# Performance work log

Hardware: AMD Instinct MI355X
Metric: run time of the kernel (lower is better)

The kernel has to match this reference:

```python
import jax, jax.numpy as jnp
import numpy as np

D_MODEL = 1024
NHEAD = 16
D_K = D_MODEL // NHEAD


def setup_inputs() -> dict:
    key = jax.random.key(0)
    ks = jax.random.split(key, 9)
    B, S = 2, 2048
    std = 1.0 / np.sqrt(D_MODEL)
    x = jax.random.normal(ks[0], (B, S, D_MODEL), dtype=jnp.float32)
    Wq = jax.random.uniform(ks[1], (D_MODEL, D_MODEL), jnp.float32, -std, std)
    bq = jax.random.uniform(ks[2], (D_MODEL,), jnp.float32, -std, std)
    Wk = jax.random.uniform(ks[3], (D_MODEL, D_MODEL), jnp.float32, -std, std)
    bk = jax.random.uniform(ks[4], (D_MODEL,), jnp.float32, -std, std)
    Wv = jax.random.uniform(ks[5], (D_MODEL, D_MODEL), jnp.float32, -std, std)
    bv = jax.random.uniform(ks[6], (D_MODEL,), jnp.float32, -std, std)
    Wo = jax.random.uniform(ks[7], (D_MODEL, D_MODEL), jnp.float32, -std, std)
    bo = jax.random.uniform(ks[8], (D_MODEL,), jnp.float32, -std, std)
    return {"x": x, "Wq": Wq, "bq": bq, "Wk": Wk, "bk": bk,
            "Wv": Wv, "bv": bv, "Wo": Wo, "bo": bo}


def reference(x, Wq, bq, Wk, bk, Wv, bv, Wo, bo):
    B, S, _ = x.shape
    scale = jnp.float32(np.sqrt(D_K))
    # Linear layers (torch nn.Linear: y = x @ W.T + b; here W stored as [in,out])
    q = (x @ Wq + bq).reshape(B, S, NHEAD, D_K).transpose(0, 2, 1, 3)  # [B,H,S,Dk]
    k = (x @ Wk + bk).reshape(B, S, NHEAD, D_K).transpose(0, 2, 1, 3)
    v = (x @ Wv + bv).reshape(B, S, NHEAD, D_K).transpose(0, 2, 1, 3)
    scores = jnp.einsum('bhqd,bhkd->bhqk', q, k) / scale  # [B,H,S,S]
    attn = jax.nn.softmax(scores, axis=-1)
    # dropout is identity in eval / deterministic reference
    out = jnp.einsum('bhqk,bhkd->bhqd', attn, v)  # [B,H,S,Dk]
    out = out.transpose(0, 2, 1, 3).reshape(B, S, D_MODEL)
    return out @ Wo + bo
```

## Files before the change

### kernel.cpp

```cpp
#include <hip/hip_runtime.h>
#include <math.h>

#define DM    1024
#define NH    16
#define DK    64
#define SLEN  2048
#define NB    2
#define MROWS (NB*SLEN)
#define QSCALE 0.1803368801111204f

typedef unsigned short u16;
typedef unsigned int   u32;
typedef short  s16x8 __attribute__((ext_vector_type(8)));
typedef _Float16 f16x8 __attribute__((ext_vector_type(8)));
typedef float  f32x4  __attribute__((ext_vector_type(4)));
typedef float  f32x16 __attribute__((ext_vector_type(16)));

#define MFMA_F16(a,b,c)   __builtin_amdgcn_mfma_f32_16x16x32_f16(a,b,c,0,0,0)
#define MFMA32_F16(a,b,c) __builtin_amdgcn_mfma_f32_32x32x16_f16(a,b,c,0,0,0)

__device__ __forceinline__ void gload16(const void* g, void* l) {
    __builtin_amdgcn_global_load_lds((const __attribute__((address_space(1))) void*)g,
                                     (__attribute__((address_space(3))) void*)l, 16, 0, 0);
}
__device__ __forceinline__ f16x8 as_h(s16x8 v) {
    union { s16x8 s; f16x8 h; } u; u.s = v; return u.h;
}
__device__ __forceinline__ float exp2_hw(float x) {
    float r; asm("v_exp_f32 %0, %1" : "=v"(r) : "v"(x)); return r;
}
__device__ __forceinline__ u32 pk2(float a, float b) {
    union { _Float16 h[2]; u32 u; } x;
    x.h[0] = (_Float16)a; x.h[1] = (_Float16)b;
    return x.u;
}
__device__ __forceinline__ void pl32swap(u32& a, u32& b) {
    asm volatile("v_permlane32_swap_b32 %0, %1" : "+v"(a), "+v"(b));
}
#define VMCNT0() asm volatile("s_waitcnt vmcnt(0)" ::: "memory")
#define BAR()    __builtin_amdgcn_s_barrier()

__global__ __launch_bounds__(256) void cvt_all(
    const float* __restrict__ x,
    const float* __restrict__ Wq, const float* __restrict__ Wk,
    const float* __restrict__ Wv, const float* __restrict__ Wo,
    _Float16* __restrict__ xh, _Float16* __restrict__ wqkv, _Float16* __restrict__ wo) {
    const int z = blockIdx.z;
    const int t = threadIdx.x;
    if (z == 4) {
        int base = (blockIdx.y * 16 + blockIdx.x) * 256 + t;
#pragma unroll
        for (int u = 0; u < 16; ++u) {
            int i = (base + u * 65536) * 4;
            float4 v = *(const float4*)&x[i];
            float vv[4] = {v.x, v.y, v.z, v.w};
            _Float16 hv[4];
#pragma unroll
            for (int j = 0; j < 4; ++j) hv[j] = (_Float16)vv[j];
            *(ushort4*)&xh[i] = *(ushort4*)hv;
        }
        return;
    }
    __shared__ _Float16 ts[64][72];
    const float* W = (z == 0) ? Wq : (z == 1) ? Wk : (z == 2) ? Wv : Wo;
    _Float16* dst = (z < 3) ? (wqkv + (size_t)z * DM * DM) : wo;
    int k0 = blockIdx.x * 64, n0 = blockIdx.y * 64;
    int kr = t >> 4, c4 = (t & 15) * 4;
#pragma unroll
    for (int u = 0; u < 4; ++u) {
        int k = kr + u * 16;
        float4 v = *(const float4*)&W[(size_t)(k0 + k) * DM + n0 + c4];
        float vv[4] = {v.x, v.y, v.z, v.w};
#pragma unroll
        for (int j = 0; j < 4; ++j) ts[c4 + j][k] = (_Float16)vv[j];
    }
    __syncthreads();
#pragma unroll
    for (int u = 0; u < 4; ++u) {
        int n = kr + u * 16;
        _Float16 hv[4];
#pragma unroll
        for (int j = 0; j < 4; ++j) hv[j] = ts[n][c4 + j];
        *(ushort4*)&dst[(size_t)(n0 + n) * DM + k0 + c4] = *(ushort4*)hv;
    }
}

template<int EPI, int BN_>
__global__ __launch_bounds__(256) void gemm_f16(
    const u16* __restrict__ Ah, const u16* __restrict__ Bt,
    const float* __restrict__ b0, const float* __restrict__ b1, const float* __restrict__ b2,
    float* __restrict__ outf, _Float16* __restrict__ qf,
    _Float16* __restrict__ kfp, _Float16* __restrict__ vtp)
{
    constexpr int NJ = BN_ / 32;
    __shared__ __align__(16) u16 sAh[2][4096];
    __shared__ __align__(16) u16 sB[2][BN_ * 32];
    const int tid = threadIdx.x, wid = tid >> 6, lane = tid & 63;
    const int lq = lane & 15, lk = lane >> 4;
    const int wm = wid >> 1, wn = wid & 1;
    const int bm = blockIdx.x * 128, bn = blockIdx.y * BN_;

    const f32x4 fz = {0.f, 0.f, 0.f, 0.f};
    f32x4 acc[4][NJ];
#pragma unroll
    for (int i = 0; i < 4; ++i)
#pragma unroll
        for (int j = 0; j < NJ; ++j) acc[i][j] = fz;

    auto stage = [&](int b, int k0) {
#pragma unroll
        for (int u = 0; u < 2; ++u) {
            int idx = u * 256 + tid, row = idx >> 2, c = (idx & 3) ^ ((row >> 1) & 3);
            size_t ga = (size_t)(bm + row) * DM + k0 + c * 8;
            gload16(Ah + ga, (char*)&sAh[b][0] + (u * 256 + wid * 64) * 16);
        }
#pragma unroll
        for (int u = 0; u < BN_ / 64; ++u) {
            int idx = u * 256 + tid, row = idx >> 2, c = (idx & 3) ^ ((row >> 1) & 3);
            size_t gb = (size_t)(bn + row) * DM + k0 + c * 8;
            gload16(Bt + gb, (char*)&sB[b][0] + (u * 256 + wid * 64) * 16);
        }
    };
    auto compute = [&](int b) {
        s16x8 avh[4], bv[NJ];
#pragma unroll
        for (int i = 0; i < 4; ++i) {
            int row = wm * 64 + i * 16 + lq;
            int off = row * 32 + ((lk ^ ((row >> 1) & 3)) << 3);
            avh[i] = *(const s16x8*)&sAh[b][off];
        }
#pragma unroll
        for (int j = 0; j < NJ; ++j) {
            int row = wn * (BN_ / 2) + j * 16 + lq;
            int off = row * 32 + ((lk ^ ((row >> 1) & 3)) << 3);
            bv[j] = *(const s16x8*)&sB[b][off];
        }
        __builtin_amdgcn_s_setprio(1);
#pragma unroll
        for (int i = 0; i < 4; ++i)
#pragma unroll
            for (int j = 0; j < NJ; ++j)
                acc[i][j] = MFMA_F16(as_h(avh[i]), as_h(bv[j]), acc[i][j]);
        __builtin_amdgcn_s_setprio(0);
    };

    int buf = 0;
    stage(0, 0);
    VMCNT0(); BAR();
    for (int t = 0; t < 31; ++t) {
        stage(buf ^ 1, (t + 1) * 32);
        compute(buf);
        VMCNT0(); BAR();
        buf ^= 1;
    }
    compute(buf);

#pragma unroll
    for (int j = 0; j < NJ; ++j) {
        int n = bn + wn * (BN_ / 2) + j * 16 + lq;
        if constexpr (EPI == 0) {
            float bias = b0[n];
#pragma unroll
            for (int i = 0; i < 4; ++i)
#pragma unroll
                for (int r = 0; r < 4; ++r) {
                    int m = bm + wm * 64 + i * 16 + lk * 4 + r;
                    outf[(size_t)m * DM + n] = acc[i][j][r] + bias;
                }
        } else {
            int mat = n >> 10, nl = n & 1023;
            int h_ = nl >> 6, d = nl & 63;
            const float* bp = (mat == 0) ? b0 : ((mat == 1) ? b1 : b2);
            float bias = bp[nl];
#pragma unroll
            for (int i = 0; i < 4; ++i) {
                int m0 = bm + wm * 64 + i * 16 + lk * 4;
                int b_ = m0 >> 11, s0 = m0 & (SLEN - 1);
                if (mat == 2) {
                    _Float16 v4[4];
#pragma unroll
                    for (int r = 0; r < 4; ++r) v4[r] = (_Float16)(acc[i][j][r] + bias);
                    *(ushort4*)&vtp[((size_t)(b_ * NH + h_) * DK + d) * SLEN + s0] = *(ushort4*)v4;
                } else {
                    _Float16* dst = (mat == 0) ? qf : kfp;
                    float sc = (mat == 0) ? QSCALE : 1.0f;
#pragma unroll
                    for (int r = 0; r < 4; ++r)
                        dst[((size_t)(b_ * NH + h_) * SLEN + s0 + r) * DK + d] =
                            (_Float16)((acc[i][j][r] + bias) * sc);
                }
            }
        }
    }
}

__global__ __launch_bounds__(256, 2) void attn_mfma(
    const _Float16* __restrict__ qf, const _Float16* __restrict__ kf,
    const _Float16* __restrict__ vt, _Float16* __restrict__ aoh)
{
    __shared__ __align__(16) _Float16 Ks[2][128 * 64];
    __shared__ __align__(16) _Float16 Vs[2][64 * 128];
    const int tid = threadIdx.x, wid = tid >> 6, lane = tid & 63;
    const int ln = lane & 31, l5 = lane >> 5;
    const int phys = blockIdx.x;
    const int virt = (phys & 7) * 64 + (phys >> 3);
    const int bh = virt >> 4, qb = virt & 15;
    const int qrow = qb * 128 + wid * 32 + ln;

    f16x8 qv[4];
#pragma unroll
    for (int t = 0; t < 4; ++t)
        qv[t] = *(const f16x8*)&qf[((size_t)bh * SLEN + qrow) * DK + t * 16 + l5 * 8];

    const _Float16* kbase = kf + (size_t)bh * SLEN * DK;
    const _Float16* vbase = vt + (size_t)bh * DK * SLEN;

    f32x16 O[2];
#pragma unroll
    for (int db = 0; db < 2; ++db)
#pragma unroll
        for (int r = 0; r < 16; ++r) O[db][r] = 0.f;
    float la0 = 0.f, la1 = 0.f, la2 = 0.f, la3 = 0.f;

    auto stage = [&](int b, int t) {
#pragma unroll
        for (int u = 0; u < 4; ++u) {
            int idx = u * 256 + tid, row = idx >> 3, c = (idx & 7) ^ (row & 7);
            gload16(kbase + (size_t)(t * 128 + row) * DK + c * 8,
                    (char*)&Ks[b][0] + (u * 256 + wid * 64) * 16);
        }
#pragma unroll
        for (int u = 0; u < 4; ++u) {
            int idx = u * 256 + tid, row = idx >> 4, c = (idx & 15) ^ (row & 15);
            gload16(vbase + (size_t)row * SLEN + t * 128 + c * 8,
                    (char*)&Vs[b][0] + (u * 256 + wid * 64) * 16);
        }
    };

    auto compute = [&](int b) {
        f32x16 S[4];
        __builtin_amdgcn_s_setprio(1);
#pragma unroll
        for (int kb = 0; kb < 4; ++kb) {
            f32x16 s;
#pragma unroll
            for (int r = 0; r < 16; ++r) s[r] = 0.f;
            int krow = kb * 32 + ln;
#pragma unroll
            for (int tp = 0; tp < 4; ++tp) {
                int cd = (2 * tp + l5) ^ (krow & 7);
                f16x8 ka = *(const f16x8*)&Ks[b][krow * 64 + cd * 8];
                s = MFMA32_F16(ka, qv[tp], s);
            }
            S[kb] = s;
        }
        __builtin_amdgcn_s_setprio(0);

        u32 pk_[4][8];
#pragma unroll
        for (int kb = 0; kb < 4; ++kb) {
#pragma unroll
            for (int i = 0; i < 8; ++i) {
                float p0 = exp2_hw(S[kb][2 * i]);
                float p1 = exp2_hw(S[kb][2 * i + 1]);
                switch (i & 3) {
                    case 0: la0 += p0 + p1; break;
                    case 1: la1 += p0 + p1; break;
                    case 2: la2 += p0 + p1; break;
                    default: la3 += p0 + p1; break;
                }
                pk_[kb][i] = pk2(p0, p1);
            }
            pl32swap(pk_[kb][0], pk_[kb][2]);
            pl32swap(pk_[kb][1], pk_[kb][3]);
            pl32swap(pk_[kb][4], pk_[kb][6]);
            pl32swap(pk_[kb][5], pk_[kb][7]);
        }

        __builtin_amdgcn_s_setprio(1);
#pragma unroll
        for (int kb = 0; kb < 4; ++kb)
#pragma unroll
            for (int t2 = 0; t2 < 2; ++t2) {
                union { u32 w[4]; f16x8 v; } pb;
#pragma unroll
                for (int w = 0; w < 4; ++w) pb.w[w] = pk_[kb][t2 * 4 + w];
#pragma unroll
                for (int db = 0; db < 2; ++db) {
                    int drow = db * 32 + ln;
                    int cd = (kb * 4 + t2 * 2 + l5) ^ (drow & 15);
                    f16x8 va = *(const f16x8*)&Vs[b][drow * 128 + cd * 8];
                    O[db] = MFMA32_F16(va, pb.v, O[db]);
                }
            }
        __builtin_amdgcn_s_setprio(0);
    };

    int buf = 0;
    stage(0, 0);
    VMCNT0(); BAR();
    for (int t = 0; t < SLEN / 128 - 1; ++t) {
        stage(buf ^ 1, t + 1);
        compute(buf);
        VMCNT0(); BAR();
        buf ^= 1;
    }
    compute(buf);

    float lp = (la0 + la1) + (la2 + la3);
    lp += __shfl_xor(lp, 32);
    float inv = 1.0f / lp;
    const int b_ = bh >> 4, h_ = bh & 15;
    size_t rowbase = ((size_t)(b_ * SLEN + qrow)) * DM + h_ * 64;
#pragma unroll
    for (int db = 0; db < 2; ++db)
#pragma unroll
        for (int u = 0; u < 4; ++u) {
            int dbase = 8 * u + 4 * l5 + 32 * db;
            _Float16 h4[4];
#pragma unroll
            for (int j = 0; j < 4; ++j) h4[j] = (_Float16)(O[db][4 * u + j] * inv);
            *(ushort4*)&aoh[rowbase + dbase] = *(ushort4*)h4;
        }
}

extern "C" void kernel_launch(void* const* d_in, const int* in_sizes, int n_in,
                              void* d_out, int out_size, void* d_ws, size_t ws_size,
                              hipStream_t stream) {
    const float* x  = (const float*)d_in[0];
    const float* Wq = (const float*)d_in[1];
    const float* bq = (const float*)d_in[2];
    const float* Wk = (const float*)d_in[3];
    const float* bk = (const float*)d_in[4];
    const float* Wv = (const float*)d_in[5];
    const float* bv = (const float*)d_in[6];
    const float* Wo = (const float*)d_in[7];
    const float* bo = (const float*)d_in[8];
    float* out = (float*)d_out;

    if (ws_size < (size_t)40 * 1024 * 1024) return;
    char* W = (char*)d_ws;
    _Float16* xh   = (_Float16*)(W);
    _Float16* wqkv = (_Float16*)(W + ((size_t)8  << 20));
    _Float16* wo   = (_Float16*)(W + ((size_t)14 << 20));
    _Float16* qf   = (_Float16*)(W + ((size_t)16 << 20));
    _Float16* kf   = (_Float16*)(W + ((size_t)24 << 20));
    _Float16* vt   = (_Float16*)(W + ((size_t)32 << 20));
    _Float16* aoh  = xh;

    cvt_all<<<dim3(16, 16, 5), dim3(256), 0, stream>>>(
        x, Wq, Wk, Wv, Wo, xh, wqkv, wo);

    gemm_f16<1, 128><<<dim3(32, 24), dim3(256), 0, stream>>>(
        (const u16*)xh, (const u16*)wqkv,
        bq, bk, bv, nullptr, qf, kf, vt);

    attn_mfma<<<dim3(512), dim3(256), 0, stream>>>(qf, kf, vt, aoh);

    gemm_f16<0, 64><<<dim3(32, 16), dim3(256), 0, stream>>>(
        (const u16*)aoh, (const u16*)wo,
        bo, nullptr, nullptr, out, nullptr, nullptr, nullptr);
}
```

Baseline: 116.2 us.

## Shrink attention blocks to two waves with 64-key tiles and retile QKV GEMM

The attention kernel now uses 128-thread blocks covering 64 query rows and streams K/V in 64-key tiles. That doubles the grid to 1024 blocks and shrinks shared memory per block. The softmax row-sum now converts to packed fp16 first and accumulates with fdot2 against ones, folding the conversion and the sum together at slightly lower precision. The QKV projection GEMM switches to a 64-wide N tile with twice as many blocks, for more parallelism at the cost of less reuse per block and more loop iterations and barriers.

Result: slower. 135.1 us (+16.2%).

```diff
diff --git a/kernel.cpp b/kernel.cpp
--- a/kernel.cpp
+++ b/kernel.cpp
@@ -12,6 +12,7 @@
 typedef unsigned short u16;
 typedef unsigned int   u32;
 typedef short  s16x8 __attribute__((ext_vector_type(8)));
+typedef __fp16 h16x2 __attribute__((ext_vector_type(2)));
 typedef _Float16 f16x8 __attribute__((ext_vector_type(8)));
 typedef float  f32x4  __attribute__((ext_vector_type(4)));
 typedef float  f32x16 __attribute__((ext_vector_type(16)));
@@ -28,11 +29,6 @@
 }
 __device__ __forceinline__ float exp2_hw(float x) {
     float r; asm("v_exp_f32 %0, %1" : "=v"(r) : "v"(x)); return r;
-}
-__device__ __forceinline__ u32 pk2(float a, float b) {
-    union { _Float16 h[2]; u32 u; } x;
-    x.h[0] = (_Float16)a; x.h[1] = (_Float16)b;
-    return x.u;
 }
 __device__ __forceinline__ void pl32swap(u32& a, u32& b) {
     asm volatile("v_permlane32_swap_b32 %0, %1" : "+v"(a), "+v"(b));
@@ -194,18 +190,17 @@
     }
 }
 
-__global__ __launch_bounds__(256, 2) void attn_mfma(
+__global__ __launch_bounds__(128, 2) void attn_mfma(
     const _Float16* __restrict__ qf, const _Float16* __restrict__ kf,
     const _Float16* __restrict__ vt, _Float16* __restrict__ aoh)
 {
-    __shared__ __align__(16) _Float16 Ks[2][128 * 64];
-    __shared__ __align__(16) _Float16 Vs[2][64 * 128];
+    __shared__ __align__(16) _Float16 Ks[2][64 * 64], Vs[2][64 * 64];
     const int tid = threadIdx.x, wid = tid >> 6, lane = tid & 63;
     const int ln = lane & 31, l5 = lane >> 5;
     const int phys = blockIdx.x;
-    const int virt = (phys & 7) * 64 + (phys >> 3);
-    const int bh = virt >> 4, qb = virt & 15;
-    const int qrow = qb * 128 + wid * 32 + ln;
+    const int virt = (phys & 7) * 128 + (phys >> 3);
+    const int bh = virt >> 5, qb = virt & 31;
+    const int qrow = qb * 64 + wid * 32 + ln;
 
     f16x8 qv[4];
 #pragma unroll
@@ -221,27 +216,23 @@
 #pragma unroll
         for (int r = 0; r < 16; ++r) O[db][r] = 0.f;
     float la0 = 0.f, la1 = 0.f, la2 = 0.f, la3 = 0.f;
+    const h16x2 ones = {(__fp16)1.0f, (__fp16)1.0f};
 
     auto stage = [&](int b, int t) {
 #pragma unroll
         for (int u = 0; u < 4; ++u) {
-            int idx = u * 256 + tid, row = idx >> 3, c = (idx & 7) ^ (row & 7);
-            gload16(kbase + (size_t)(t * 128 + row) * DK + c * 8,
-                    (char*)&Ks[b][0] + (u * 256 + wid * 64) * 16);
-        }
-#pragma unroll
-        for (int u = 0; u < 4; ++u) {
-            int idx = u * 256 + tid, row = idx >> 4, c = (idx & 15) ^ (row & 15);
-            gload16(vbase + (size_t)row * SLEN + t * 128 + c * 8,
-                    (char*)&Vs[b][0] + (u * 256 + wid * 64) * 16);
+            int idx = u * 128 + tid, row = idx >> 3, c = (idx & 7) ^ (row & 7);
+            int lo = (u * 128 + wid * 64) * 16;
+            gload16(kbase + (size_t)(t * 64 + row) * DK + c * 8, (char*)&Ks[b][0] + lo);
+            gload16(vbase + (size_t)row * SLEN + t * 64 + c * 8, (char*)&Vs[b][0] + lo);
         }
     };
 
     auto compute = [&](int b) {
-        f32x16 S[4];
+        f32x16 S[2];
         __builtin_amdgcn_s_setprio(1);
 #pragma unroll
-        for (int kb = 0; kb < 4; ++kb) {
+        for (int kb = 0; kb < 2; ++kb) {
             f32x16 s;
 #pragma unroll
             for (int r = 0; r < 16; ++r) s[r] = 0.f;
@@ -256,20 +247,22 @@
         }
         __builtin_amdgcn_s_setprio(0);
 
-        u32 pk_[4][8];
-#pragma unroll
-        for (int kb = 0; kb < 4; ++kb) {
+        u32 pk_[2][8];
+#pragma unroll
+        for (int kb = 0; kb < 2; ++kb) {
 #pragma unroll
             for (int i = 0; i < 8; ++i) {
                 float p0 = exp2_hw(S[kb][2 * i]);
                 float p1 = exp2_hw(S[kb][2 * i + 1]);
+                h16x2 pk = __builtin_amdgcn_cvt_pkrtz(p0, p1);
                 switch (i & 3) {
-                    case 0: la0 += p0 + p1; break;
-                    case 1: la1 += p0 + p1; break;
-                    case 2: la2 += p0 + p1; break;
-                    default: la3 += p0 + p1; break;
+                    case 0: la0 = __builtin_amdgcn_fdot2(pk, ones, la0, false); break;
+                    case 1: la1 = __builtin_amdgcn_fdot2(pk, ones, la1, false); break;
+                    case 2: la2 = __builtin_amdgcn_fdot2(pk, ones, la2, false); break;
+                    default: la3 = __builtin_amdgcn_fdot2(pk, ones, la3, false); break;
                 }
-                pk_[kb][i] = pk2(p0, p1);
+                union { h16x2 h; u32 u; } cv; cv.h = pk;
+                pk_[kb][i] = cv.u;
             }
             pl32swap(pk_[kb][0], pk_[kb][2]);
             pl32swap(pk_[kb][1], pk_[kb][3]);
@@ -279,7 +272,7 @@
 
         __builtin_amdgcn_s_setprio(1);
 #pragma unroll
-        for (int kb = 0; kb < 4; ++kb)
+        for (int kb = 0; kb < 2; ++kb)
 #pragma unroll
             for (int t2 = 0; t2 < 2; ++t2) {
                 union { u32 w[4]; f16x8 v; } pb;
@@ -288,8 +281,9 @@
 #pragma unroll
                 for (int db = 0; db < 2; ++db) {
                     int drow = db * 32 + ln;
-                    int cd = (kb * 4 + t2 * 2 + l5) ^ (drow & 15);
-                    f16x8 va = *(const f16x8*)&Vs[b][drow * 128 + cd * 8];
+                    int seg = kb * 2 + t2;
+                    int ch = (seg * 2 + l5) ^ (drow & 7);
+                    f16x8 va = *(const f16x8*)&Vs[b][drow * 64 + ch * 8];
                     O[db] = MFMA32_F16(va, pb.v, O[db]);
                 }
             }
@@ -299,7 +293,7 @@
     int buf = 0;
     stage(0, 0);
     VMCNT0(); BAR();
-    for (int t = 0; t < SLEN / 128 - 1; ++t) {
+    for (int t = 0; t < SLEN / 64 - 1; ++t) {
         stage(buf ^ 1, t + 1);
         compute(buf);
         VMCNT0(); BAR();
@@ -351,11 +345,11 @@
     cvt_all<<<dim3(16, 16, 5), dim3(256), 0, stream>>>(
         x, Wq, Wk, Wv, Wo, xh, wqkv, wo);
 
-    gemm_f16<1, 128><<<dim3(32, 24), dim3(256), 0, stream>>>(
+    gemm_f16<1, 64><<<dim3(32, 48), dim3(256), 0, stream>>>(
         (const u16*)xh, (const u16*)wqkv,
         bq, bk, bv, nullptr, qf, kf, vt);
 
-    attn_mfma<<<dim3(512), dim3(256), 0, stream>>>(qf, kf, vt, aoh);
+    attn_mfma<<<dim3(1024), dim3(128), 0, stream>>>(qf, kf, vt, aoh);
 
     gemm_f16<0, 64><<<dim3(32, 16), dim3(256), 0, stream>>>(
         (const u16*)aoh, (const u16*)wo,
```
